# Kernel tuning notes

Measured on AMD Instinct MI355X. Metric: run time of the kernel, lower is better.

The kernel has to match this reference:

```python
import jax, jax.numpy as jnp
import numpy as np

IRREPS = [0, 1, 2, 3, 4]   # l values; dim = sum(2l+1) = 25
MAX_L = max(IRREPS)
DIM = sum(2 * l + 1 for l in IRREPS)
EPS = 1e-14
N_POINTS = 200000


def _p_terms(i, a, b, l):
    """Ivanic-Ruedenberg P(i,l,a,b) as sparse terms: (coef, flat idx into R1 (3x3), flat idx into D^{l-1})."""
    lp = l - 1
    n = 2 * lp + 1
    row = i + 1  # R1 rows/cols indexed by m in {-1,0,1} -> {0,1,2}
    if b == l:
        return [(1.0, row * 3 + 2, (a + lp) * n + 2 * lp),
                (-1.0, row * 3 + 0, (a + lp) * n + 0)]
    if b == -l:
        return [(1.0, row * 3 + 2, (a + lp) * n + 0),
                (1.0, row * 3 + 0, (a + lp) * n + 2 * lp)]
    return [(1.0, row * 3 + 1, (a + lp) * n + (b + lp))]


def _ru_tables(l):
    """Precompute sparse recurrence tables for building D^l from D^{l-1} and R1."""
    out_idx, rij, ab, coef = [], [], [], []
    n = 2 * l + 1
    for m in range(-l, l + 1):
        for mp in range(-l, l + 1):
            denom = (2 * l) * (2 * l - 1) if abs(mp) == l else (l + mp) * (l - mp)
            d0 = 1.0 if m == 0 else 0.0
            u = np.sqrt((l + m) * (l - m) / denom)
            v = 0.5 * np.sqrt((1 + d0) * (l + abs(m) - 1) * (l + abs(m)) / denom) * (1 - 2 * d0)
            w = -0.5 * np.sqrt(max(l - abs(m) - 1, 0) * (l - abs(m)) / denom) * (1 - d0)
            terms = []
            if u != 0.0:
                terms += [(u * c, i, j) for c, i, j in _p_terms(0, m, mp, l)]
            if v != 0.0:
                if m == 0:
                    terms += [(v * c, i, j) for c, i, j in _p_terms(1, 1, mp, l)]
                    terms += [(v * c, i, j) for c, i, j in _p_terms(-1, -1, mp, l)]
                elif m > 0:
                    s = np.sqrt(2.0) if m == 1 else 1.0
                    terms += [(v * s * c, i, j) for c, i, j in _p_terms(1, m - 1, mp, l)]
                    if m != 1:
                        terms += [(-v * c, i, j) for c, i, j in _p_terms(-1, -m + 1, mp, l)]
                else:
                    if m != -1:
                        terms += [(v * c, i, j) for c, i, j in _p_terms(1, m + 1, mp, l)]
                    s = np.sqrt(2.0) if m == -1 else 1.0
                    terms += [(v * s * c, i, j) for c, i, j in _p_terms(-1, -m - 1, mp, l)]
            if w != 0.0:
                if m > 0:
                    terms += [(w * c, i, j) for c, i, j in _p_terms(1, m + 1, mp, l)]
                    terms += [(w * c, i, j) for c, i, j in _p_terms(-1, -m - 1, mp, l)]
                else:
                    terms += [(w * c, i, j) for c, i, j in _p_terms(1, m - 1, mp, l)]
                    terms += [(-w * c, i, j) for c, i, j in _p_terms(-1, -m + 1, mp, l)]
            o = (m + l) * n + (mp + l)
            for c, i, j in terms:
                out_idx.append(o); rij.append(i); ab.append(j); coef.append(c)
    return (np.asarray(out_idx), np.asarray(rij), np.asarray(ab),
            np.asarray(coef, dtype=np.float32))


_TABLES = {l: _ru_tables(l) for l in range(2, MAX_L + 1)}


def _wigner_blocks(R1, max_l):
    """D^l for real spherical harmonics via Ivanic-Ruedenberg recurrence. R1: (N,3,3)."""
    N = R1.shape[0]
    blocks = {0: jnp.ones((N, 1, 1), R1.dtype), 1: R1}
    r1f = R1.reshape(N, 9)
    for l in range(2, max_l + 1):
        oi, rij, ab, cf = _TABLES[l]
        dprev = blocks[l - 1].reshape(N, (2 * l - 1) ** 2)
        contrib = cf[None, :] * r1f[:, rij] * dprev[:, ab]  # (N, n_terms)
        n = 2 * l + 1
        Dl = jnp.zeros((N, n * n), R1.dtype).at[:, oi].add(contrib)
        blocks[l] = Dl.reshape(N, n, n)
    return blocks


def _forward(xyz):
    # angles of v (normalized=True): theta polar, phi azimuthal
    norm = jnp.linalg.norm(xyz, axis=-1, keepdims=True)
    v = xyz / jnp.maximum(norm, EPS)
    ct = jnp.clip(v[..., 2], -1.0, 1.0)
    theta = jnp.arccos(ct)
    phi = jnp.arctan2(v[..., 1], v[..., 0])
    st, cp, sp = jnp.sin(theta), jnp.cos(phi), jnp.sin(phi)
    z = jnp.zeros_like(ct)
    # R = Ry(-theta) @ Rz(-phi): R @ v = |v| z_hat
    R = jnp.stack([
        jnp.stack([ct * cp, ct * sp, -st], -1),
        jnp.stack([-sp, cp, z], -1),
        jnp.stack([st * cp, st * sp, ct], -1),
    ], -2)  # (N,3,3)
    # real-SH l=1 basis order m=(-1,0,1) <-> (y,z,x)
    p = jnp.array([1, 2, 0])
    R1 = R[:, p][:, :, p]
    blocks = _wigner_blocks(R1, MAX_L)
    N = xyz.shape[0]
    D = jnp.zeros((N, DIM, DIM), xyz.dtype)
    off = 0
    for l in IRREPS:
        d = 2 * l + 1
        D = D.at[:, off:off + d, off:off + d].set(blocks[l])
        off += d
    return D


def setup_inputs() -> dict:
    key = jax.random.key(0)
    xyz = jax.random.normal(key, (N_POINTS, 3), dtype=jnp.float32)
    return {"xyz": xyz}


def reference(xyz):
    return _forward(xyz)
```

## Files before the change

### kernel.cpp

```cpp
#include <hip/hip_runtime.h>
#include <utility>
#include <cstddef>


struct Term { int o; int r; int a; float c; };
struct LTable { int n; Term t[1024]; };

constexpr double csqrt(double x) {
    if (x <= 0.0) return 0.0;
    double g = x < 1.0 ? 1.0 : x;
    for (int i = 0; i < 50; ++i) g = 0.5 * (g + x / g);
    return g;
}
constexpr int cabs_i(int x) { return x < 0 ? -x : x; }
constexpr int cmax_i(int a, int b) { return a > b ? a : b; }

constexpr void add_p(LTable& T, int o, double scale, int i, int a, int b, int l) {
    int lp = l - 1;
    int np = 2 * lp + 1;
    int row = i + 1;
    if (b == l) {
        T.t[T.n++] = Term{o, row * 3 + 2, (a + lp) * np + 2 * lp, (float)scale};
        T.t[T.n++] = Term{o, row * 3 + 0, (a + lp) * np + 0,      (float)(-scale)};
    } else if (b == -l) {
        T.t[T.n++] = Term{o, row * 3 + 2, (a + lp) * np + 0,      (float)scale};
        T.t[T.n++] = Term{o, row * 3 + 0, (a + lp) * np + 2 * lp, (float)scale};
    } else {
        T.t[T.n++] = Term{o, row * 3 + 1, (a + lp) * np + (b + lp), (float)scale};
    }
}

constexpr LTable ru_table(int l) {
    LTable T{};
    int n = 2 * l + 1;
    for (int m = -l; m <= l; ++m) {
        for (int mp = -l; mp <= l; ++mp) {
            double denom = (cabs_i(mp) == l) ? (double)((2 * l) * (2 * l - 1))
                                             : (double)((l + mp) * (l - mp));
            double d0 = (m == 0) ? 1.0 : 0.0;
            double u = csqrt((double)((l + m) * (l - m)) / denom);
            double v = 0.5 * csqrt((1.0 + d0) * (l + cabs_i(m) - 1) * (l + cabs_i(m)) / denom)
                       * (1.0 - 2.0 * d0);
            double w = -0.5 * csqrt((double)cmax_i(l - cabs_i(m) - 1, 0) * (l - cabs_i(m)) / denom)
                       * (1.0 - d0);
            int o = (m + l) * n + (mp + l);
            if (u != 0.0) add_p(T, o, u, 0, m, mp, l);
            if (v != 0.0) {
                if (m == 0) {
                    add_p(T, o, v, 1, 1, mp, l);
                    add_p(T, o, v, -1, -1, mp, l);
                } else if (m > 0) {
                    double s = (m == 1) ? csqrt(2.0) : 1.0;
                    add_p(T, o, v * s, 1, m - 1, mp, l);
                    if (m != 1) add_p(T, o, -v, -1, -m + 1, mp, l);
                } else {
                    if (m != -1) add_p(T, o, v, 1, m + 1, mp, l);
                    double s = (m == -1) ? csqrt(2.0) : 1.0;
                    add_p(T, o, v * s, -1, -m - 1, mp, l);
                }
            }
            if (w != 0.0) {
                if (m > 0) {
                    add_p(T, o, w, 1, m + 1, mp, l);
                    add_p(T, o, w, -1, -m - 1, mp, l);
                } else {
                    add_p(T, o, w, 1, m - 1, mp, l);
                    add_p(T, o, -w, -1, -m + 1, mp, l);
                }
            }
        }
    }
    return T;
}

inline constexpr LTable T2 = ru_table(2);
inline constexpr LTable T3 = ru_table(3);
inline constexpr LTable T4 = ru_table(4);

template<const LTable& T>
constexpr int er_start(int e) {
    for (int i = 0; i < T.n; ++i) if (T.t[i].o == e) return i;
    return 0;
}
template<const LTable& T>
constexpr int er_cnt(int e) {
    int c = 0;
    for (int i = 0; i < T.n; ++i) if (T.t[i].o == e) ++c;
    return c;
}

template<const LTable& T, int S, size_t... K>
__device__ __forceinline__ float sum_terms(const float* __restrict__ R1,
                                           const float* __restrict__ P,
                                           std::index_sequence<K...>) {
    float a = 0.0f;
    ((a = fmaf(T.t[S + (int)K].c, R1[T.t[S + (int)K].r] * P[T.t[S + (int)K].a], a)), ...);
    return a;
}

template<const LTable& T, int l, bool KEEP, int e>
__device__ __forceinline__ void level_one(const float* __restrict__ R1,
                                          const float* __restrict__ P,
                                          float* __restrict__ keep,
                                          float* __restrict__ row) {
    constexpr int S = er_start<T>(e);
    constexpr int C = er_cnt<T>(e);
    float v = sum_terms<T, S>(R1, P, std::make_index_sequence<C>{});
    if constexpr (KEEP) keep[e] = v;
    constexpr int d = 2 * l + 1;
    constexpr int r = e / d, c = e % d;
    constexpr int E625 = (l * l + r) * 25 + (l * l + c);
    row[E625] = v;
}

template<const LTable& T, int l, bool KEEP, size_t... E>
__device__ __forceinline__ void level(const float* __restrict__ R1,
                                      const float* __restrict__ P,
                                      float* __restrict__ keep,
                                      float* __restrict__ row,
                                      std::index_sequence<E...>) {
    (level_one<T, l, KEEP, (int)E>(R1, P, keep, row), ...);
}

template<size_t... E>
__device__ __forceinline__ void write_l1(const float* __restrict__ D1,
                                         float* __restrict__ row,
                                         std::index_sequence<E...>) {
    ((row[(1 + (int)E / 3) * 25 + (1 + (int)E % 3)] = D1[E]), ...);
}

typedef float v4f __attribute__((ext_vector_type(4)));


__global__ __launch_bounds__(256, 2)
void wigner_fused_kernel(const float* __restrict__ xyz, float* __restrict__ out, int Ntot) {
    __shared__ float img[32 * 625];

    const int t = threadIdx.x;
    const int gp = blockIdx.x * 256 + t;

    float x = 0.0f, y = 0.0f, z = 1.0f;
    if (gp < Ntot) {
        x = xyz[3 * gp + 0];
        y = xyz[3 * gp + 1];
        z = xyz[3 * gp + 2];
    }

    const float r2 = x * x + y * y + z * z;
    const float rinv = rsqrtf(fmaxf(r2, 1e-24f));
    const float ct = fminf(fmaxf(z * rinv, -1.0f), 1.0f);
    const float st = sqrtf(fmaxf(1.0f - ct * ct, 0.0f));
    const float rxy2 = x * x + y * y;
    float cp = 1.0f, sp = 0.0f;
    if (rxy2 > 0.0f) {
        const float ri = rsqrtf(rxy2);
        cp = x * ri;
        sp = y * ri;
    }

    v4f* b4 = (v4f*)img;
    const v4f z4 = {0.0f, 0.0f, 0.0f, 0.0f};
#pragma unroll 4
    for (int k = t; k < 5000; k += 256) b4[k] = z4;
    __syncthreads();

    const int p0 = t & 31;
    const long long blk_f = (long long)blockIdx.x * 256 * 625;

    for (int c = 0; c < 8; ++c) {
        const int base_pt = blockIdx.x * 256 + c * 32;
        if (base_pt >= Ntot) break;
        const int vp = min(32, Ntot - base_pt);

        if ((t >> 5) == c && gp < Ntot) {
            float* __restrict__ row = img + p0 * 625;
            row[0] = 1.0f;

            float D1[9] = {cp,      0.0f, -sp,
                           st * sp, ct,   st * cp,
                           ct * sp, -st,  ct * cp};
            write_l1(D1, row, std::make_index_sequence<9>{});

            float D2[25];
            level<T2, 2, true>(D1, D1, D2, row, std::make_index_sequence<25>{});
            float D3[49];
            level<T3, 3, true>(D1, D2, D3, row, std::make_index_sequence<49>{});
            level<T4, 4, false>(D1, D3, nullptr, row, std::make_index_sequence<81>{});
        }
        __syncthreads();

        const long long out_f = blk_f + (long long)c * 32 * 625;
        if (vp == 32) {
            const v4f* src = (const v4f*)img;
            v4f* dst = (v4f*)(out + out_f);
#pragma unroll 4
            for (int k = t; k < 5000; k += 256) {
                __builtin_nontemporal_store(src[k], dst + k);
            }
        } else {
            const int vf = vp * 625;
            for (int k = t; k < vf; k += 256) {
                out[out_f + k] = img[k];
            }
        }
        __syncthreads();
    }
}

extern "C" void kernel_launch(void* const* d_in, const int* in_sizes, int n_in,
                              void* d_out, int out_size, void* d_ws, size_t ws_size,
                              hipStream_t stream) {
    const float* xyz = (const float*)d_in[0];
    float* out = (float*)d_out;
    const int N = in_sizes[0] / 3;
    const int blocks = (N + 255) / 256;
    hipLaunchKernelGGL(wigner_fused_kernel, dim3(blocks), dim3(256), 0, stream,
                       xyz, out, N);
}
```

Measured before the change: 538.6 us.

## Double-buffer LDS staging so compute of next chunk overlaps store of previous

Splits the shared-memory image into two 16-point buffers and software-pipelines the loop: in each iteration all threads stream the previous chunk to global memory while 16 threads compute the next chunk into the other buffer. This halves the synchronisations per point pair and overlaps the serial per-chunk compute with the global stores. The trade-off is that only 16 lanes compute at a time, so the compute is more serialized across 16 chunks. Zero entries stay valid because both buffers are zeroed once and the same off-diagonal slots are never written.

```diff
diff --git a/kernel.cpp b/kernel.cpp
--- a/kernel.cpp
+++ b/kernel.cpp
@@ -134,7 +134,7 @@
 
 __global__ __launch_bounds__(256, 2)
 void wigner_fused_kernel(const float* __restrict__ xyz, float* __restrict__ out, int Ntot) {
-    __shared__ float img[32 * 625];
+    __shared__ float buf[2][16 * 625];
 
     const int t = threadIdx.x;
     const int gp = blockIdx.x * 256 + t;
@@ -158,22 +158,44 @@
         sp = y * ri;
     }
 
-    v4f* b4 = (v4f*)img;
-    const v4f z4 = {0.0f, 0.0f, 0.0f, 0.0f};
+    {
+        v4f* b4 = (v4f*)&buf[0][0];
+        const v4f z4 = {0.0f, 0.0f, 0.0f, 0.0f};
 #pragma unroll 4
-    for (int k = t; k < 5000; k += 256) b4[k] = z4;
+        for (int k = t; k < 5000; k += 256) b4[k] = z4;
+    }
     __syncthreads();
 
-    const int p0 = t & 31;
+    const int p0 = t & 15;
+    const int own = t >> 4;
     const long long blk_f = (long long)blockIdx.x * 256 * 625;
 
-    for (int c = 0; c < 8; ++c) {
-        const int base_pt = blockIdx.x * 256 + c * 32;
-        if (base_pt >= Ntot) break;
-        const int vp = min(32, Ntot - base_pt);
-
-        if ((t >> 5) == c && gp < Ntot) {
-            float* __restrict__ row = img + p0 * 625;
+#pragma unroll 1
+    for (int c = 0; c <= 16; ++c) {
+        if (c > 0) {
+            const int pc = c - 1;
+            const int pbase = blockIdx.x * 256 + pc * 16;
+            if (pbase < Ntot) {
+                const int vp = min(16, Ntot - pbase);
+                const long long out_f = blk_f + (long long)pc * 16 * 625;
+                if (vp == 16) {
+                    const v4f* src = (const v4f*)&buf[pc & 1][0];
+                    v4f* dst = (v4f*)(out + out_f);
+                    for (int k = t; k < 2500; k += 256) {
+                        __builtin_nontemporal_store(src[k], dst + k);
+                    }
+                } else {
+                    const float* srcf = &buf[pc & 1][0];
+                    const int vf = vp * 625;
+                    for (int k = t; k < vf; k += 256) {
+                        out[out_f + k] = srcf[k];
+                    }
+                }
+            }
+        }
+
+        if (c < 16 && own == c && gp < Ntot) {
+            float* __restrict__ row = &buf[c & 1][0] + p0 * 625;
             row[0] = 1.0f;
 
             float D1[9] = {cp,      0.0f, -sp,
@@ -187,22 +209,7 @@
             level<T3, 3, true>(D1, D2, D3, row, std::make_index_sequence<49>{});
             level<T4, 4, false>(D1, D3, nullptr, row, std::make_index_sequence<81>{});
         }
-        __syncthreads();
-
-        const long long out_f = blk_f + (long long)c * 32 * 625;
-        if (vp == 32) {
-            const v4f* src = (const v4f*)img;
-            v4f* dst = (v4f*)(out + out_f);
-#pragma unroll 4
-            for (int k = t; k < 5000; k += 256) {
-                __builtin_nontemporal_store(src[k], dst + k);
-            }
-        } else {
-            const int vf = vp * 625;
-            for (int k = t; k < vf; k += 256) {
-                out[out_f + k] = img[k];
-            }
-        }
+
         __syncthreads();
     }
 }
```

Result: no change. 544.4 us (+1.1%).
